# Kernel tuning notes

Measured on AMD Instinct MI355X. Metric: run time of the kernel, lower is better.

The kernel has to match this reference:

```python
import jax, jax.numpy as jnp
import numpy as np

EMA_DECAY = 0.99
NUM_EXPERTS = 64
N_TOKENS = 2097152
TOP_K = 4


def setup_inputs() -> dict:
    key = jax.random.key(0)
    k1, k2, k3 = jax.random.split(key, 3)
    expert_indices = jax.random.randint(k1, (N_TOKENS, TOP_K), 0, NUM_EXPERTS, dtype=jnp.int64)
    expert_weights = jax.random.uniform(k2, (N_TOKENS, TOP_K), dtype=jnp.float32)
    expert_load_ema = jax.random.uniform(k3, (NUM_EXPERTS,), dtype=jnp.float32)
    expert_pair_coactivation = jnp.zeros((NUM_EXPERTS, NUM_EXPERTS), dtype=jnp.float32)
    return {
        "expert_indices": expert_indices,
        "expert_weights": expert_weights,
        "expert_load_ema": expert_load_ema,
        "expert_pair_coactivation": expert_pair_coactivation,
    }


def reference(expert_indices, expert_weights, expert_load_ema, expert_pair_coactivation):
    # expert_indices: [N, K] int; buffers: [E], [E, E]
    N, K = expert_indices.shape
    E = expert_load_ema.shape[0]

    # --- load histogram: sum over all top-k slots, normalize by N ---
    flat = expert_indices.reshape(-1)  # [N*K]
    counts = jnp.zeros((E,), dtype=expert_load_ema.dtype).at[flat].add(1.0)
    load = counts / max(N, 1)

    # EMA update of per-expert load
    new_load_ema = expert_load_ema * EMA_DECAY + load * (1.0 - EMA_DECAY)

    # --- pairwise co-activation histogram over all (k1 < k2) column pairs ---
    k1s, k2s = np.triu_indices(K, k=1)  # static pair enumeration
    a = expert_indices[:, k1s].reshape(-1)  # [N * K*(K-1)/2]
    b = expert_indices[:, k2s].reshape(-1)
    new_coact = (
        expert_pair_coactivation
        .at[a, b].add(1.0)
        .at[b, a].add(1.0)
    )

    return new_load_ema, new_coact
```

## Files before the change

kernel.cpp:

```cpp
#include <hip/hip_runtime.h>


#define N_TOKENS    2097152
#define NUM_EXPERTS 64
#define NCELLS      (NUM_EXPERTS * NUM_EXPERTS)
#define NBLOCKS     512
#define NTHREADS    512
#define STRIDE      (NBLOCKS * NTHREADS)

__device__ __forceinline__ void pair_add(int* s, int a, int b) {
    const int lo = min(a, b), hi = max(a, b);
    atomicAdd(&s[(lo << 6) + (hi ^ (lo & 31))], 1);
}

__device__ __forceinline__ void token_add(int* s, int4 v) {
    pair_add(s, v.x, v.y);
    pair_add(s, v.x, v.z);
    pair_add(s, v.x, v.w);
    pair_add(s, v.y, v.z);
    pair_add(s, v.y, v.w);
    pair_add(s, v.z, v.w);
}

__global__ __launch_bounds__(NTHREADS) void coact_accum_kernel(
    const int* __restrict__ idx, int* __restrict__ ws)
{
    __shared__ int s_coact[NCELLS];
    for (int i = threadIdx.x; i < NCELLS; i += NTHREADS) s_coact[i] = 0;
    __syncthreads();

    const int tid = blockIdx.x * NTHREADS + threadIdx.x;
    const int4* __restrict__ idx4 = (const int4*)idx;

    int4 v[8];
    #pragma unroll
    for (int i = 0; i < 8; ++i) v[i] = idx4[tid + i * STRIDE];

    __builtin_amdgcn_sched_barrier(0);

    #pragma unroll
    for (int i = 0; i < 8; ++i) token_add(s_coact, v[i]);

    __syncthreads();

    for (int i = threadIdx.x; i < NCELLS; i += NTHREADS) {
        int c = s_coact[i];
        if (c) {
            const int lo = i >> 6;
            const int hi = (i & 63) ^ (lo & 31);
            atomicAdd(&ws[(lo << 6) + hi], c);
        }
    }
}

__global__ __launch_bounds__(256) void finalize_kernel(
    const int* __restrict__ ws,
    const float* __restrict__ ema_in,
    const float* __restrict__ coact_in,
    float* __restrict__ out)
{
    const int t = threadIdx.x;

    for (int c = t; c < NCELLS; c += 256) {
        const int i = c >> 6, j = c & 63;
        const int lo = min(i, j), hi = max(i, j);
        int d = ws[(lo << 6) + hi];
        if (i == j) d *= 2;
        out[NUM_EXPERTS + c] = coact_in[c] + (float)d;
    }

    if (t < NUM_EXPERTS) {
        int rowsum = 0;
        #pragma unroll
        for (int j = 0; j < NUM_EXPERTS; ++j) {
            const int lo = min(t, j), hi = max(t, j);
            int d = ws[(lo << 6) + hi];
            rowsum += (j == t) ? 2 * d : d;
        }
        const int count = rowsum / 3;
        const float load = (float)count / (float)N_TOKENS;
        out[t] = ema_in[t] * 0.99f + load * 0.01f;
    }
}

extern "C" void kernel_launch(void* const* d_in, const int* in_sizes, int n_in,
                              void* d_out, int out_size, void* d_ws, size_t ws_size,
                              hipStream_t stream)
{
    const int*   idx      = (const int*)d_in[0];
    const float* ema_in   = (const float*)d_in[2];
    const float* coact_in = (const float*)d_in[3];
    float*       out      = (float*)d_out;
    int*         ws       = (int*)d_ws;

    hipMemsetAsync(ws, 0, NCELLS * sizeof(int), stream);

    coact_accum_kernel<<<NBLOCKS, NTHREADS, 0, stream>>>(idx, ws);
    finalize_kernel<<<1, 256, 0, stream>>>(ws, ema_in, coact_in, out);
}
```

Measured before the change: 106.9 us.

## Replace global atomics with per-block partial slices and parallel finalize reduction

Each accumulation block now writes its full shared-memory histogram plus per-expert row sums into its own workspace slice instead of atomically adding into one global histogram. This removes the workspace memset and the global atomic contention. A 64-block finalize kernel then reduces the 512 slices column by column and computes the EMA from the precomputed row sums. The cost is about 8 MB of extra workspace writes and reads, plus a heavier finalize pass.

```diff
diff --git a/kernel.cpp b/kernel.cpp
--- a/kernel.cpp
+++ b/kernel.cpp
@@ -7,6 +7,7 @@
 #define NBLOCKS     512
 #define NTHREADS    512
 #define STRIDE      (NBLOCKS * NTHREADS)
+#define SLICE       (NCELLS + NUM_EXPERTS)
 
 __device__ __forceinline__ void pair_add(int* s, int a, int b) {
     const int lo = min(a, b), hi = max(a, b);
@@ -26,7 +27,9 @@
     const int* __restrict__ idx, int* __restrict__ ws)
 {
     __shared__ int s_coact[NCELLS];
+    __shared__ int s_row[NUM_EXPERTS];
     for (int i = threadIdx.x; i < NCELLS; i += NTHREADS) s_coact[i] = 0;
+    if (threadIdx.x < NUM_EXPERTS) s_row[threadIdx.x] = 0;
     __syncthreads();
 
     const int tid = blockIdx.x * NTHREADS + threadIdx.x;
@@ -35,7 +38,6 @@
     int4 v[8];
     #pragma unroll
     for (int i = 0; i < 8; ++i) v[i] = idx4[tid + i * STRIDE];
-
     __builtin_amdgcn_sched_barrier(0);
 
     #pragma unroll
@@ -43,43 +45,83 @@
 
     __syncthreads();
 
-    for (int i = threadIdx.x; i < NCELLS; i += NTHREADS) {
-        int c = s_coact[i];
-        if (c) {
-            const int lo = i >> 6;
-            const int hi = (i & 63) ^ (lo & 31);
-            atomicAdd(&ws[(lo << 6) + hi], c);
+    {
+        const int e = threadIdx.x & 63;
+        const int c = threadIdx.x >> 6;
+        int p = 0;
+        #pragma unroll
+        for (int k = 0; k < 8; ++k) {
+            const int j = c * 8 + k;
+            int u;
+            if (j >= e) {
+                u = s_coact[(e << 6) + (j ^ (e & 31))];
+                if (j == e) u <<= 1;
+            } else {
+                u = s_coact[(j << 6) + (e ^ (j & 31))];
+            }
+            p += u;
         }
+        atomicAdd(&s_row[e], p);
+    }
+    __syncthreads();
+
+    int* slice = ws + blockIdx.x * SLICE;
+    const int4* sc4 = (const int4*)s_coact;
+    int4* dst4 = (int4*)slice;
+    dst4[threadIdx.x * 2]     = sc4[threadIdx.x * 2];
+    dst4[threadIdx.x * 2 + 1] = sc4[threadIdx.x * 2 + 1];
+    if (threadIdx.x < NUM_EXPERTS / 4) {
+        ((int4*)(slice + NCELLS))[threadIdx.x] = ((const int4*)s_row)[threadIdx.x];
     }
 }
 
-__global__ __launch_bounds__(256) void finalize_kernel(
+__global__ __launch_bounds__(512) void finalize_kernel(
     const int* __restrict__ ws,
     const float* __restrict__ ema_in,
     const float* __restrict__ coact_in,
     float* __restrict__ out)
 {
+    __shared__ int red[512];
+    __shared__ int rowf[NUM_EXPERTS];
+    __shared__ int s_rowsum;
+    const int b = blockIdx.x;
     const int t = threadIdx.x;
+    if (t == 0) s_rowsum = 0;
 
-    for (int c = t; c < NCELLS; c += 256) {
-        const int i = c >> 6, j = c & 63;
-        const int lo = min(i, j), hi = max(i, j);
-        int d = ws[(lo << 6) + hi];
-        if (i == j) d *= 2;
-        out[NUM_EXPERTS + c] = coact_in[c] + (float)d;
-    }
+    const int ema_part = ws[t * SLICE + NCELLS + b];
+
+    const int g = t >> 6, lane = t & 63;
+    int acc = 0;
+    #pragma unroll 8
+    for (int s = g * 64; s < g * 64 + 64; ++s)
+        acc += ws[s * SLICE + b * 64 + lane];
+    red[t] = acc;
+    __syncthreads();
 
     if (t < NUM_EXPERTS) {
-        int rowsum = 0;
+        int v = 0;
         #pragma unroll
-        for (int j = 0; j < NUM_EXPERTS; ++j) {
-            const int lo = min(t, j), hi = max(t, j);
-            int d = ws[(lo << 6) + hi];
-            rowsum += (j == t) ? 2 * d : d;
+        for (int gg = 0; gg < 8; ++gg) v += red[gg * 64 + t];
+        rowf[t] = v;
+    }
+    atomicAdd(&s_rowsum, ema_part);
+    __syncthreads();
+
+    if (t < NUM_EXPERTS) {
+        const int j = t;
+        if (j > b) {
+            const float d = (float)rowf[j ^ (b & 31)];
+            out[NUM_EXPERTS + b * 64 + j] = coact_in[b * 64 + j] + d;
+            out[NUM_EXPERTS + j * 64 + b] = coact_in[j * 64 + b] + d;
+        } else if (j == b) {
+            out[NUM_EXPERTS + b * 65] =
+                coact_in[b * 65] + 2.0f * (float)rowf[b ^ (b & 31)];
         }
-        const int count = rowsum / 3;
+    }
+    if (t == 0) {
+        const int count = s_rowsum / 3;
         const float load = (float)count / (float)N_TOKENS;
-        out[t] = ema_in[t] * 0.99f + load * 0.01f;
+        out[b] = ema_in[b] * 0.99f + load * 0.01f;
     }
 }
 
@@ -93,8 +135,6 @@
     float*       out      = (float*)d_out;
     int*         ws       = (int*)d_ws;
 
-    hipMemsetAsync(ws, 0, NCELLS * sizeof(int), stream);
-
     coact_accum_kernel<<<NBLOCKS, NTHREADS, 0, stream>>>(idx, ws);
-    finalize_kernel<<<1, 256, 0, stream>>>(ws, ema_in, coact_in, out);
+    finalize_kernel<<<NUM_EXPERTS, 512, 0, stream>>>(ws, ema_in, coact_in, out);
 }
```

After: 102.7 us. -3.9%, faster.
